# Optimization experiments

Measured on AMD Instinct MI355X. Metric: run time of the kernel, lower is better.

## Reference

```python
import jax, jax.numpy as jnp
import numpy as np

B, S, D, H = 4, 2048, 1024, 16
DK = D // H


def setup_inputs() -> dict:
    key = jax.random.key(0)
    ks = jax.random.split(key, 11)
    scale = 1.0 / np.sqrt(D)
    inp = {
        "query": jax.random.normal(ks[0], (B, S, D), jnp.float32),
        "key": jax.random.normal(ks[1], (B, S, D), jnp.float32),
        "value": jax.random.normal(ks[2], (B, S, D), jnp.float32),
    }
    # 4 linear layers: Wq, Wk, Wv, Wo (torch Linear: y = x @ W.T + b)
    for i, name in enumerate(["q", "k", "v", "o"]):
        inp[f"W{name}"] = jax.random.uniform(ks[3 + 2 * i], (D, D), jnp.float32, -scale, scale)
        inp[f"b{name}"] = jax.random.uniform(ks[4 + 2 * i], (D,), jnp.float32, -scale, scale)
    return inp


def reference(query, key, value, Wq, bq, Wk, bk, Wv, bv, Wo, bo):
    def proj(x, W, b):
        # [B,S,D] -> [B,H,S,DK]
        y = x @ W.T + b
        return y.reshape(B, S, H, DK).transpose(0, 2, 1, 3)

    q = proj(query, Wq, bq)
    k = proj(key, Wk, bk)
    v = proj(value, Wv, bv)
    scores = jnp.einsum("bhqd,bhkd->bhqk", q, k) / jnp.sqrt(jnp.float32(DK))
    p = jax.nn.softmax(scores, axis=-1)  # dropout p=0 -> identity
    ctx = jnp.einsum("bhqk,bhkd->bhqd", p, v)
    ctx = ctx.transpose(0, 2, 1, 3).reshape(B, S, D)
    return ctx @ Wo.T + bo
```

## Files before the change

### kernel.cpp

```cpp
#include <hip/hip_runtime.h>

typedef unsigned short u16;
typedef unsigned int u32;
typedef __attribute__((ext_vector_type(8))) short short8v;
typedef __attribute__((ext_vector_type(4))) short short4v;
typedef __attribute__((ext_vector_type(4))) float floatx4;

#define BB 4
#define SS 2048
#define DD 1024
#define HH 16
#define DKK 64
#define MM (BB * SS)
#define KK DD
#define NN DD
#define QSCALE 0.18033688011112042f

#define PS_RS 12
#define PS_CS 200
#define PS_REGION 1600

__device__ __forceinline__ u16 f2bf(float f) {
  union { __bf16 h; u16 u; } r; r.h = (__bf16)f; return r.u;
}
__device__ __forceinline__ u32 pack2bf(float a, float b) {
  union { u32 u; __bf16 h[2]; } r;
  r.h[0] = (__bf16)a; r.h[1] = (__bf16)b; return r.u;
}
__device__ __forceinline__ short8v cat44(short4v a, short4v b) {
  return __builtin_shufflevector(a, b, 0, 1, 2, 3, 4, 5, 6, 7);
}

__device__ __forceinline__ void load_lds16(const void* g, void* l) {
  __builtin_amdgcn_global_load_lds((const __attribute__((address_space(1))) void*)g,
                                   (__attribute__((address_space(3))) void*)l, 16, 0, 0);
}

__device__ __forceinline__ floatx4 mfma_k32(short8v a, short8v b, floatx4 c) {
  return __builtin_amdgcn_mfma_f32_16x16x32_bf16(a, b, c, 0, 0, 0);
}

__global__ __launch_bounds__(256) void cvt_w4(const float* __restrict__ w0,
                                              const float* __restrict__ w1,
                                              const float* __restrict__ w2,
                                              const float* __restrict__ w3,
                                              u16* __restrict__ out) {
  const int y = blockIdx.y;
  const float* in = (y == 0) ? w0 : (y == 1) ? w1 : (y == 2) ? w2 : w3;
  u16* o = out + (size_t)y * DD * DD;
  const int i = (blockIdx.x * 256 + threadIdx.x) * 8;
  float4 a = *(const float4*)(in + i);
  float4 b = *(const float4*)(in + i + 4);
  uint4 v;
  v.x = pack2bf(a.x, a.y); v.y = pack2bf(a.z, a.w);
  v.z = pack2bf(b.x, b.y); v.w = pack2bf(b.z, b.w);
  *(uint4*)(o + i) = v;
}

__global__ __launch_bounds__(256) void cvt_a3(const float* __restrict__ a0,
                                              const float* __restrict__ a1,
                                              const float* __restrict__ a2,
                                              u16* __restrict__ o0, u16* __restrict__ o1,
                                              u16* __restrict__ o2) {
  const int y = blockIdx.y;
  const float* in = (y == 0) ? a0 : (y == 1) ? a1 : a2;
  u16* o = (y == 0) ? o0 : (y == 1) ? o1 : o2;
  const int i = (blockIdx.x * 256 + threadIdx.x) * 8;
  float4 a = *(const float4*)(in + i);
  float4 b = *(const float4*)(in + i + 4);
  uint4 v;
  v.x = pack2bf(a.x, a.y); v.y = pack2bf(a.z, a.w);
  v.z = pack2bf(b.x, b.y); v.w = pack2bf(b.z, b.w);
  *(uint4*)(o + i) = v;
}

#define NT (KK / 64)
#define ITERS (NT / 2)

__device__ __forceinline__ void stage_half(const u16* __restrict__ gsrc, u16* ldst,
                                           int tid) {
#pragma unroll
  for (int L = 0; L < 2; ++L) {
    const int s = L * 512 + tid;
    const int r = s >> 3;
    const int g = (s & 7) ^ (r & 7);
    load_lds16(gsrc + (size_t)r * KK + g * 8, ldst + s * 8);
  }
}

__device__ __forceinline__ void gemm256_core(const u16* __restrict__ A,
                                             const u16* __restrict__ W,
                                             u16* As, u16* Bs,
                                             floatx4 (&acc)[8][4]) {
  const int tid = threadIdx.x;
  const int w = tid >> 6, lane = tid & 63;
  const int wm = w >> 2, wn = w & 3;
  const int wnh = wn >> 1, wno = wn & 1;
  const int lr = lane & 15;
  const int c0 = (((lane >> 2) & 1) << 5) | ((((lane >> 4) ^ lane) & 3) << 3);

#define AP(d, fr, kk) \
  (*(const short8v*)(As + ((d)*2 + wm) * 8192 + ((fr)*16 + lr) * 64 + (c0 ^ ((kk)*32))))
#define BP(d, fc, kk) \
  (*(const short8v*)(Bs + ((d)*2 + wnh) * 8192 + (wno * 64 + (fc)*16 + lr) * 64 + (c0 ^ ((kk)*32))))
#define MFMA8(FROFF, B, FCOFF)                                                  \
  _Pragma("unroll") for (int fr_ = 0; fr_ < 4; ++fr_)                           \
  _Pragma("unroll") for (int fc_ = 0; fc_ < 2; ++fc_) {                         \
    acc[(FROFF) + fr_][(FCOFF) + fc_] =                                         \
        mfma_k32(a[fr_][0], B[fc_][0], acc[(FROFF) + fr_][(FCOFF) + fc_]);      \
    acc[(FROFF) + fr_][(FCOFF) + fc_] =                                         \
        mfma_k32(a[fr_][1], B[fc_][1], acc[(FROFF) + fr_][(FCOFF) + fc_]);      \
  }
#define BAR() __builtin_amdgcn_s_barrier()
#define PRIO1() __builtin_amdgcn_s_setprio(1)
#define PRIO0() __builtin_amdgcn_s_setprio(0)

  short8v a[4][2], b01[2][2], b23[2][2];

  stage_half(A, As + 0 * 8192, tid);
  stage_half(A + (size_t)128 * KK, As + 1 * 8192, tid);
  stage_half(W, Bs + 0 * 8192, tid);
  stage_half(W + (size_t)128 * KK, Bs + 1 * 8192, tid);
  stage_half(W + 64, Bs + 2 * 8192, tid);
  stage_half(W + (size_t)128 * KK + 64, Bs + 3 * 8192, tid);
  asm volatile("s_waitcnt vmcnt(4)" ::: "memory");
  BAR();

#pragma unroll 1
  for (int j = 0; j < ITERS; ++j) {
    const int e = 2 * j, o = e + 1;
    const bool haveE2 = (j + 1 < ITERS);
#pragma unroll
    for (int fr = 0; fr < 4; ++fr) { a[fr][0] = AP(0, fr, 0); a[fr][1] = AP(0, fr, 1); }
#pragma unroll
    for (int fc = 0; fc < 2; ++fc) { b01[fc][0] = BP(0, fc, 0); b01[fc][1] = BP(0, fc, 1); }
    stage_half(A + (size_t)o * 64, As + 2 * 8192, tid);
    BAR(); PRIO1(); MFMA8(0, b01, 0); PRIO0(); BAR();
#pragma unroll
    for (int fc = 0; fc < 2; ++fc) { b23[fc][0] = BP(0, fc + 2, 0); b23[fc][1] = BP(0, fc + 2, 1); }
    stage_half(A + (size_t)128 * KK + (size_t)o * 64, As + 3 * 8192, tid);
    BAR(); PRIO1(); MFMA8(0, b23, 2); PRIO0(); BAR();
#pragma unroll
    for (int fr = 0; fr < 4; ++fr) { a[fr][0] = AP(0, fr + 4, 0); a[fr][1] = AP(0, fr + 4, 1); }
    if (haveE2) stage_half(W + (size_t)(e + 2) * 64, Bs + 0 * 8192, tid);
    BAR(); PRIO1(); MFMA8(4, b01, 0); PRIO0(); BAR();
    if (haveE2) {
      stage_half(W + (size_t)128 * KK + (size_t)(e + 2) * 64, Bs + 1 * 8192, tid);
      asm volatile("s_waitcnt vmcnt(4)" ::: "memory");
    } else {
      asm volatile("s_waitcnt vmcnt(0)" ::: "memory");
    }
    BAR(); PRIO1(); MFMA8(4, b23, 2); PRIO0(); BAR();
#pragma unroll
    for (int fr = 0; fr < 4; ++fr) { a[fr][0] = AP(1, fr, 0); a[fr][1] = AP(1, fr, 1); }
#pragma unroll
    for (int fc = 0; fc < 2; ++fc) { b01[fc][0] = BP(1, fc, 0); b01[fc][1] = BP(1, fc, 1); }
    if (haveE2) stage_half(A + (size_t)(e + 2) * 64, As + 0 * 8192, tid);
    BAR(); PRIO1(); MFMA8(0, b01, 0); PRIO0(); BAR();
#pragma unroll
    for (int fc = 0; fc < 2; ++fc) { b23[fc][0] = BP(1, fc + 2, 0); b23[fc][1] = BP(1, fc + 2, 1); }
    if (haveE2) stage_half(A + (size_t)128 * KK + (size_t)(e + 2) * 64, As + 1 * 8192, tid);
    BAR(); PRIO1(); MFMA8(0, b23, 2); PRIO0(); BAR();
#pragma unroll
    for (int fr = 0; fr < 4; ++fr) { a[fr][0] = AP(1, fr + 4, 0); a[fr][1] = AP(1, fr + 4, 1); }
    if (haveE2) stage_half(W + (size_t)(o + 2) * 64, Bs + 2 * 8192, tid);
    BAR(); PRIO1(); MFMA8(4, b01, 0); PRIO0(); BAR();
    if (haveE2) {
      stage_half(W + (size_t)128 * KK + (size_t)(o + 2) * 64, Bs + 3 * 8192, tid);
      asm volatile("s_waitcnt vmcnt(4)" ::: "memory");
    }
    BAR(); PRIO1(); MFMA8(4, b23, 2); PRIO0(); BAR();
  }
#undef AP
#undef BP
#undef MFMA8
#undef BAR
#undef PRIO1
#undef PRIO0
}

__global__ __launch_bounds__(512, 2) void proj_gemm(
    const u16* __restrict__ qc, const u16* __restrict__ kc, const u16* __restrict__ vc,
    const u16* __restrict__ Wq, const u16* __restrict__ Wk, const u16* __restrict__ Wv,
    const float* __restrict__ bq, const float* __restrict__ bk, const float* __restrict__ bv,
    u16* __restrict__ Qb, u16* __restrict__ Kb, u16* __restrict__ Vtb) {
  __shared__ __align__(16) u16 As[2 * 2 * 8192];
  __shared__ __align__(16) u16 Bs[2 * 2 * 8192];
  const int z = blockIdx.z;
  const u16* A = (z == 0) ? qc : (z == 1) ? kc : vc;
  const u16* W = (z == 0) ? Wq : (z == 1) ? Wk : Wv;
  const float* bias = (z == 0) ? bq : (z == 1) ? bk : bv;
  const int m0 = blockIdx.x * 256, n0 = blockIdx.y * 256;

  floatx4 acc[8][4] = {};
  gemm256_core(A + (size_t)m0 * KK, W + (size_t)n0 * KK, As, Bs, acc);

  const int tid = threadIdx.x;
  const int w = tid >> 6, lane = tid & 63;
  const int lr = lane & 15, lq = lane >> 4;
  const int wm = w >> 2, wn = w & 3;
  const int row0 = m0 + wm * 128;
  const int col0 = n0 + wn * 64;

  if (z == 2) {
#pragma unroll
    for (int fc = 0; fc < 4; ++fc) {
      const int col = col0 + fc * 16 + lr;
      const float bv_ = bias[col];
      const int h = col >> 6, dk = col & 63;
#pragma unroll
      for (int fr = 0; fr < 8; ++fr) {
        const int row = row0 + fr * 16 + lq * 4;
        const int b = row >> 11, s = row & (SS - 1);
        uint2 pk;
        pk.x = pack2bf(acc[fr][fc][0] + bv_, acc[fr][fc][1] + bv_);
        pk.y = pack2bf(acc[fr][fc][2] + bv_, acc[fr][fc][3] + bv_);
        *(uint2*)&Vtb[(((size_t)(b * HH + h)) * DKK + dk) * SS + s] = pk;
      }
    }
  } else {
    u16* out = (z == 0) ? Qb : Kb;
    const float sc = (z == 0) ? QSCALE : 1.0f;
#pragma unroll
    for (int fc = 0; fc < 4; ++fc) {
      const int col = col0 + fc * 16 + lr;
      const float bv_ = bias[col];
#pragma unroll
      for (int fr = 0; fr < 8; ++fr)
#pragma unroll
        for (int rr = 0; rr < 4; ++rr) {
          const int row = row0 + fr * 16 + lq * 4 + rr;
          out[(size_t)row * NN + col] = f2bf((acc[fr][fc][rr] + bv_) * sc);
        }
    }
  }
}

__global__ __launch_bounds__(512, 2) void out_gemm(const u16* __restrict__ A,
                                                   const u16* __restrict__ W,
                                                   const float* __restrict__ bias,
                                                   float* __restrict__ out) {
  __shared__ __align__(16) u16 As[2 * 2 * 8192];
  __shared__ __align__(16) u16 Bs[2 * 2 * 8192];
  const int m0 = blockIdx.x * 256, n0 = blockIdx.y * 256;
  floatx4 acc[8][4] = {};
  gemm256_core(A + (size_t)m0 * KK, W + (size_t)n0 * KK, As, Bs, acc);

  const int tid = threadIdx.x;
  const int w = tid >> 6, lane = tid & 63;
  const int lr = lane & 15, lq = lane >> 4;
  const int wm = w >> 2, wn = w & 3;
  const int row0 = m0 + wm * 128;
  const int col0 = n0 + wn * 64;
#pragma unroll
  for (int fc = 0; fc < 4; ++fc) {
    const int col = col0 + fc * 16 + lr;
    const float bv = bias[col];
#pragma unroll
    for (int fr = 0; fr < 8; ++fr)
#pragma unroll
      for (int rr = 0; rr < 4; ++rr) {
        const int row = row0 + fr * 16 + lq * 4 + rr;
        out[(size_t)row * NN + col] = acc[fr][fc][rr] + bv;
      }
  }
}

__global__ __launch_bounds__(256, 4) void attn_kernel(const u16* __restrict__ Q,
                                                      const u16* __restrict__ Kmat,
                                                      const u16* __restrict__ Vt,
                                                      u16* __restrict__ ctx) {
  __shared__ __align__(16) u16 Ks[64 * 64];
  __shared__ __align__(16) u16 Vs[64 * 64];
  __shared__ __align__(16) u16 Ps[4 * PS_REGION];
  const int tid = threadIdx.x;
  const int w = tid >> 6, lane = tid & 63;
  const int lr = lane & 15, lq = lane >> 4;
  const int bh = blockIdx.x, b = bh >> 4, h = bh & 15;
  const int q0 = blockIdx.y * 128;

  short8v qf[2][2];
  {
    const u16* qp = Q + ((size_t)(b * SS + q0 + w * 32 + lr)) * DD + h * 64 + lq * 8;
    qf[0][0] = *(const short8v*)qp;
    qf[0][1] = *(const short8v*)(qp + 32);
    qf[1][0] = *(const short8v*)(qp + 16 * DD);
    qf[1][1] = *(const short8v*)(qp + 16 * DD + 32);
  }
  floatx4 o[2][4] = {};
  float l_part[2][4] = {};

  const u16* kp = Kmat + ((size_t)(b * SS + w * 16 + lr)) * DD + h * 64 + lq * 8;
  const u16* vp = Vt + (((size_t)(b * HH + h)) * DKK + w * 16 + lr) * SS + lq * 8;

  for (int kt = 0; kt < SS / 64; ++kt) {
    load_lds16(kp,      &Ks[(2 * w) * 512]);
    load_lds16(kp + 32, &Ks[(2 * w + 1) * 512]);
    load_lds16(vp,      &Vs[(2 * w) * 512]);
    load_lds16(vp + 32, &Vs[(2 * w + 1) * 512]);
    kp += 64 * DD; vp += 64;
    __syncthreads();

    floatx4 sc[2][4] = {};
#pragma unroll
    for (int t = 0; t < 4; ++t) {
      short8v kb0 = *(const short8v*)&Ks[t * 1024 + lane * 8];
      short8v kb1 = *(const short8v*)&Ks[t * 1024 + 512 + lane * 8];
#pragma unroll
      for (int s = 0; s < 2; ++s) {
        sc[s][t] = mfma_k32(qf[s][0], kb0, sc[s][t]);
        sc[s][t] = mfma_k32(qf[s][1], kb1, sc[s][t]);
      }
    }

    short8v pa[2][2];
#pragma unroll
    for (int s = 0; s < 2; ++s) {
#pragma unroll
      for (int t = 0; t < 4; ++t) {
#pragma unroll
        for (int r = 0; r < 4; ++r) {
          const float e = __builtin_amdgcn_exp2f(sc[s][t][r]);
          sc[s][t][r] = e;
          l_part[s][r] += e;
        }
      }
      u16* pw = &Ps[w * PS_REGION];
#pragma unroll
      for (int t = 0; t < 4; ++t) {
        const int base = (2 * t + (lr >> 3)) * PS_CS + (lr & 7);
#pragma unroll
        for (int r = 0; r < 4; ++r)
          pw[base + (lq * 4 + r) * PS_RS] = f2bf(sc[s][t][r]);
      }
      {
        const u16* rp0 = pw + lq * PS_CS + lr * PS_RS;
        const u16* rp1 = pw + (4 + lq) * PS_CS + lr * PS_RS;
        pa[s][0] = cat44(*(const short4v*)rp0, *(const short4v*)(rp0 + 4));
        pa[s][1] = cat44(*(const short4v*)rp1, *(const short4v*)(rp1 + 4));
      }
    }

#pragma unroll
    for (int t = 0; t < 4; ++t) {
      short8v vb0 = *(const short8v*)&Vs[t * 1024 + lane * 8];
      short8v vb1 = *(const short8v*)&Vs[t * 1024 + 512 + lane * 8];
#pragma unroll
      for (int s = 0; s < 2; ++s) {
        o[s][t] = mfma_k32(pa[s][0], vb0, o[s][t]);
        o[s][t] = mfma_k32(pa[s][1], vb1, o[s][t]);
      }
    }
    __syncthreads();
  }

  float inv[2][4];
#pragma unroll
  for (int s = 0; s < 2; ++s)
#pragma unroll
    for (int r = 0; r < 4; ++r) {
      float l = l_part[s][r];
      l += __shfl_xor(l, 1); l += __shfl_xor(l, 2);
      l += __shfl_xor(l, 4); l += __shfl_xor(l, 8);
      inv[s][r] = 1.0f / l;
    }

#pragma unroll
  for (int s = 0; s < 2; ++s)
#pragma unroll
    for (int r = 0; r < 4; ++r) {
      const int sq = q0 + w * 32 + s * 16 + lq * 4 + r;
      u16* cp = ctx + ((size_t)(b * SS + sq)) * DD + h * 64;
      const float iv = inv[s][r];
#pragma unroll
      for (int t = 0; t < 4; ++t)
        cp[t * 16 + lr] = f2bf(o[s][t][r] * iv);
    }
}

extern "C" void kernel_launch(void* const* d_in, const int* in_sizes, int n_in,
                              void* d_out, int out_size, void* d_ws, size_t ws_size,
                              hipStream_t stream) {
  const float* query = (const float*)d_in[0];
  const float* key   = (const float*)d_in[1];
  const float* value = (const float*)d_in[2];
  const float* Wq = (const float*)d_in[3];  const float* bq = (const float*)d_in[4];
  const float* Wk = (const float*)d_in[5];  const float* bk = (const float*)d_in[6];
  const float* Wv = (const float*)d_in[7];  const float* bv = (const float*)d_in[8];
  const float* Wo = (const float*)d_in[9];  const float* bo = (const float*)d_in[10];
  float* out = (float*)d_out;

  char* ws = (char*)d_ws;
  size_t off = 0;
  u16* Wb   = (u16*)(ws + off); off += (size_t)4 * DD * DD * 2;
  u16* Qb   = (u16*)(ws + off); off += (size_t)MM * DD * 2;
  u16* Kb   = (u16*)(ws + off); off += (size_t)MM * DD * 2;
  u16* Vtb  = (u16*)(ws + off); off += (size_t)MM * DD * 2;
  u16* qc   = (u16*)(ws + off);
  u16* ctxb = qc;               off += (size_t)MM * DD * 2;
  u16* kc = (u16*)d_out;
  u16* vc = (u16*)d_out + (size_t)MM * DD;
  u16* Wq_b = Wb, *Wk_b = Wb + (size_t)DD * DD, *Wv_b = Wb + (size_t)2 * DD * DD,
     *Wo_b = Wb + (size_t)3 * DD * DD;

  const int wn = DD * DD, an = MM * DD;
  cvt_w4<<<dim3(wn / 2048, 4), 256, 0, stream>>>(Wq, Wk, Wv, Wo, Wb);
  cvt_a3<<<dim3(an / 2048, 3), 256, 0, stream>>>(query, key, value, qc, kc, vc);

  proj_gemm<<<dim3(MM / 256, NN / 256, 3), 512, 0, stream>>>(
      qc, kc, vc, Wq_b, Wk_b, Wv_b, bq, bk, bv, Qb, Kb, Vtb);

  attn_kernel<<<dim3(BB * HH, SS / 128), 256, 0, stream>>>(Qb, Kb, Vtb, ctxb);

  out_gemm<<<dim3(MM / 256, NN / 256), 512, 0, stream>>>(ctxb, Wo_b, bo, out);
}
```

Measured before the change: 363.2 us.

## Double-buffer K tiles in attention and overlap V loads with QK compute

The attention loop now double-buffers the K tile in LDS, prefetching the next K tile while the current one is consumed. V loads are issued early and waited on only before the PV MFMAs, using explicit vmcnt waits and raw barriers instead of __syncthreads. It also raises wave priority around the MFMA sections. This aims to hide global-to-LDS latency behind compute, at the cost of more LDS (an extra 8KB), which may reduce occupancy, and of fragile hand-counted vmcnt values.

```diff
diff --git a/kernel.cpp b/kernel.cpp
--- a/kernel.cpp
+++ b/kernel.cpp
@@ -270,7 +270,7 @@
                                                       const u16* __restrict__ Kmat,
                                                       const u16* __restrict__ Vt,
                                                       u16* __restrict__ ctx) {
-  __shared__ __align__(16) u16 Ks[64 * 64];
+  __shared__ __align__(16) u16 Ks[2][64 * 64];
   __shared__ __align__(16) u16 Vs[64 * 64];
   __shared__ __align__(16) u16 Ps[4 * PS_REGION];
   const int tid = threadIdx.x;
@@ -293,25 +293,41 @@
   const u16* kp = Kmat + ((size_t)(b * SS + w * 16 + lr)) * DD + h * 64 + lq * 8;
   const u16* vp = Vt + (((size_t)(b * HH + h)) * DKK + w * 16 + lr) * SS + lq * 8;
 
+  load_lds16(kp,      &Ks[0][(2 * w) * 512]);
+  load_lds16(kp + 32, &Ks[0][(2 * w + 1) * 512]);
+  kp += 64 * DD;
+
+#pragma unroll 1
   for (int kt = 0; kt < SS / 64; ++kt) {
-    load_lds16(kp,      &Ks[(2 * w) * 512]);
-    load_lds16(kp + 32, &Ks[(2 * w + 1) * 512]);
+    const int bf = kt & 1;
+    const bool haveNext = (kt + 1 < SS / 64);
+    __builtin_amdgcn_s_barrier();
     load_lds16(vp,      &Vs[(2 * w) * 512]);
     load_lds16(vp + 32, &Vs[(2 * w + 1) * 512]);
-    kp += 64 * DD; vp += 64;
-    __syncthreads();
+    vp += 64;
+    if (haveNext) {
+      load_lds16(kp,      &Ks[bf ^ 1][(2 * w) * 512]);
+      load_lds16(kp + 32, &Ks[bf ^ 1][(2 * w + 1) * 512]);
+      kp += 64 * DD;
+      asm volatile("s_waitcnt vmcnt(4)" ::: "memory");
+    } else {
+      asm volatile("s_waitcnt vmcnt(2)" ::: "memory");
+    }
+    __builtin_amdgcn_s_barrier();
 
     floatx4 sc[2][4] = {};
+    __builtin_amdgcn_s_setprio(1);
 #pragma unroll
     for (int t = 0; t < 4; ++t) {
-      short8v kb0 = *(const short8v*)&Ks[t * 1024 + lane * 8];
-      short8v kb1 = *(const short8v*)&Ks[t * 1024 + 512 + lane * 8];
+      short8v kb0 = *(const short8v*)&Ks[bf][t * 1024 + lane * 8];
+      short8v kb1 = *(const short8v*)&Ks[bf][t * 1024 + 512 + lane * 8];
 #pragma unroll
       for (int s = 0; s < 2; ++s) {
         sc[s][t] = mfma_k32(qf[s][0], kb0, sc[s][t]);
         sc[s][t] = mfma_k32(qf[s][1], kb1, sc[s][t]);
       }
     }
+    __builtin_amdgcn_s_setprio(0);
 
     short8v pa[2][2];
 #pragma unroll
@@ -341,6 +357,14 @@
       }
     }
 
+    if (haveNext) {
+      asm volatile("s_waitcnt vmcnt(2)" ::: "memory");
+    } else {
+      asm volatile("s_waitcnt vmcnt(0)" ::: "memory");
+    }
+    __builtin_amdgcn_s_barrier();
+
+    __builtin_amdgcn_s_setprio(1);
 #pragma unroll
     for (int t = 0; t < 4; ++t) {
       short8v vb0 = *(const short8v*)&Vs[t * 1024 + lane * 8];
@@ -351,7 +375,7 @@
         o[s][t] = mfma_k32(pa[s][1], vb1, o[s][t]);
       }
     }
-    __syncthreads();
+    __builtin_amdgcn_s_setprio(0);
   }
 
   float inv[2][4];
```

Result: faster. 342.1 us (-5.8%).
